# Optimization experiments

Hardware: AMD Instinct MI355X
Metric: run time of the kernel (lower is better)

Reference implementation:

```python
import jax, jax.numpy as jnp
import numpy as np

D_MODEL = 64  # per-head dim used for temperature


def setup_inputs() -> dict:
    key = jax.random.key(0)
    kq, kk, kv, km = jax.random.split(key, 4)
    B, S, D = 16, 2048, D_MODEL
    q = jax.random.normal(kq, (B, S, D), dtype=jnp.float32)
    k = jax.random.normal(kk, (B, S, D), dtype=jnp.float32)
    v = jax.random.normal(kv, (B, S, D), dtype=jnp.float32)
    attn_mask = jax.random.randint(km, (B, S), 0, 2).astype(bool)  # True = masked
    return {"q": q, "k": k, "v": v, "attn_mask": attn_mask}


def reference(q, k, v, attn_mask):
    temper = jnp.asarray(D_MODEL ** 0.5, dtype=q.dtype)
    # scores: [B, S_q, S_k]
    attn = jnp.einsum('bqd,bkd->bqk', q, k) / temper
    # mask broadcast over query dim (torch: unsqueeze(1).expand_as)
    attn = jnp.where(attn_mask[:, None, :], -jnp.inf, attn)
    attn = jax.nn.softmax(attn, axis=-1)
    # nan-fix: fully-masked rows produce NaN -> set to 0 (matches torch code)
    attn = jnp.where(jnp.isnan(attn), jnp.zeros((), dtype=attn.dtype), attn)
    # dropout prob is 0.0 -> identity
    output = jnp.einsum('bqk,bkd->bqd', attn, v)
    return (output, attn)
```

## Files before the change

### kernel.cpp

```cpp
#include <hip/hip_runtime.h>
#include <math.h>

constexpr int B = 16, S = 2048, D = 64;
constexpr int TQ = 128;
constexpr int TK = 64;
constexpr int NT = S / TK;
constexpr float SCALE = 0.125f;
constexpr int STR = 72;

typedef __attribute__((ext_vector_type(8))) short bf16x8;
typedef __attribute__((ext_vector_type(16))) float f32x16;

__device__ __forceinline__ unsigned short f2bf(float x) {
    union { float f; unsigned u; } c; c.f = x;
    return (unsigned short)((c.u + 0x7fff + ((c.u >> 16) & 1)) >> 16);
}
__device__ __forceinline__ float bf2f(unsigned short h) {
    union { unsigned u; float f; } c; c.u = ((unsigned)h) << 16; return c.f;
}
__device__ __forceinline__ unsigned pk2(float a, float b) {
    return (unsigned)f2bf(a) | ((unsigned)f2bf(b) << 16);
}

__global__ __launch_bounds__(256)
void sdpa_mfma(const float* __restrict__ qg, const float* __restrict__ kg,
               const float* __restrict__ vg, const int* __restrict__ maskg,
               float* __restrict__ outg, float* __restrict__ attng)
{
    __shared__ __align__(16) short Qs[TQ * STR];
    __shared__ __align__(16) short Ks[TK * STR];
    __shared__ __align__(16) short Vt[D * STR];
    __shared__ __align__(16) short Ps[4 * 32 * STR];
    __shared__ float mflag[TK];

    const int t = threadIdx.x;
    const int w = t >> 6, lane = t & 63, m = lane & 31, half = lane >> 5;
    const int b = blockIdx.x >> 4;
    const int q0 = (blockIdx.x & 15) * TQ;

    {
        const float4* src = (const float4*)(qg + ((size_t)b * S + q0) * D);
        #pragma unroll
        for (int i = 0; i < 8; ++i) {
            int f4 = t + i * 256;
            float4 v = src[f4];
            int r = f4 >> 4, c = (f4 & 15) * 4;
            unsigned* dst = (unsigned*)&Qs[r * STR + c];
            dst[0] = pk2(v.x, v.y); dst[1] = pk2(v.z, v.w);
        }
    }
    __syncthreads();

    bf16x8 aq[4];
    #pragma unroll
    for (int s = 0; s < 4; ++s)
        aq[s] = *(const bf16x8*)&Qs[(w * 32 + m) * STR + s * 16 + half * 8];

    auto stageK = [&](int gk) {
        const float4* src = (const float4*)(kg + ((size_t)b * S + gk) * D);
        #pragma unroll
        for (int i = 0; i < 4; ++i) {
            int f4 = t + i * 256;
            float4 v = src[f4];
            int r = f4 >> 4, c = (f4 & 15) * 4;
            unsigned* dst = (unsigned*)&Ks[r * STR + c];
            dst[0] = pk2(v.x, v.y); dst[1] = pk2(v.z, v.w);
        }
        if (t < TK) mflag[t] = maskg[b * S + gk + t] ? 1.0f : 0.0f;
    };
    auto stageV = [&](int gk) {
        const float4* src = (const float4*)(vg + ((size_t)b * S + gk) * D);
        #pragma unroll
        for (int i = 0; i < 4; ++i) {
            int f4 = t + i * 256;
            float4 v = src[f4];
            int r = f4 >> 4, c = (f4 & 15) * 4;
            Vt[(c + 0) * STR + r] = (short)f2bf(v.x);
            Vt[(c + 1) * STR + r] = (short)f2bf(v.y);
            Vt[(c + 2) * STR + r] = (short)f2bf(v.z);
            Vt[(c + 3) * STR + r] = (short)f2bf(v.w);
        }
    };
    auto scores = [&](f32x16& c0, f32x16& c1) {
        #pragma unroll
        for (int i = 0; i < 16; ++i) { c0[i] = 0.f; c1[i] = 0.f; }
        #pragma unroll
        for (int s = 0; s < 4; ++s) {
            bf16x8 b0 = *(const bf16x8*)&Ks[m * STR + s * 16 + half * 8];
            bf16x8 b1 = *(const bf16x8*)&Ks[(32 + m) * STR + s * 16 + half * 8];
            c0 = __builtin_amdgcn_mfma_f32_32x32x16_bf16(aq[s], b0, c0, 0, 0, 0);
            c1 = __builtin_amdgcn_mfma_f32_32x32x16_bf16(aq[s], b1, c1, 0, 0, 0);
        }
    };

    float rs[16];
    #pragma unroll
    for (int r = 0; r < 16; ++r) rs[r] = 0.f;

    for (int tile = 0; tile < NT; ++tile) {
        stageK(tile * TK);
        __syncthreads();
        f32x16 c0, c1; scores(c0, c1);
        float mk0 = mflag[m], mk1 = mflag[32 + m];
        #pragma unroll
        for (int r = 0; r < 16; ++r) {
            float p0 = (mk0 == 0.f) ? __expf(c0[r] * SCALE) : 0.f;
            float p1 = (mk1 == 0.f) ? __expf(c1[r] * SCALE) : 0.f;
            rs[r] += p0 + p1;
        }
        __syncthreads();
    }
    #pragma unroll
    for (int off = 1; off < 32; off <<= 1)
        #pragma unroll
        for (int r = 0; r < 16; ++r) rs[r] += __shfl_xor(rs[r], off, 64);
    float rli[16];
    #pragma unroll
    for (int r = 0; r < 16; ++r) rli[r] = rs[r] > 0.f ? 1.f / rs[r] : 0.f;

    f32x16 o0, o1;
    #pragma unroll
    for (int i = 0; i < 16; ++i) { o0[i] = 0.f; o1[i] = 0.f; }
    short* Pw = &Ps[w * 32 * STR];
    float* abase = attng + ((size_t)(b * S + q0 + w * 32)) * S;

    for (int tile = 0; tile < NT; ++tile) {
        const int gk = tile * TK;
        stageK(gk); stageV(gk);
        __syncthreads();
        f32x16 c0, c1; scores(c0, c1);
        float mk0 = mflag[m], mk1 = mflag[32 + m];
        #pragma unroll
        for (int r = 0; r < 16; ++r) {
            int row = (r & 3) + 8 * (r >> 2) + 4 * half;
            float p0 = (mk0 == 0.f) ? __expf(c0[r] * SCALE) * rli[r] : 0.f;
            float p1 = (mk1 == 0.f) ? __expf(c1[r] * SCALE) * rli[r] : 0.f;
            Pw[row * STR + m]      = (short)f2bf(p0);
            Pw[row * STR + 32 + m] = (short)f2bf(p1);
        }
        #pragma unroll
        for (int i = 0; i < 16; ++i) {
            int row = i * 2 + half;
            unsigned u = *(const unsigned*)&Pw[row * STR + 2 * m];
            float2 val = make_float2(bf2f((unsigned short)(u & 0xffff)),
                                     bf2f((unsigned short)(u >> 16)));
            *(float2*)&abase[(size_t)row * S + gk + 2 * m] = val;
        }
        #pragma unroll
        for (int kk = 0; kk < 4; ++kk) {
            bf16x8 ap  = *(const bf16x8*)&Pw[m * STR + kk * 16 + half * 8];
            bf16x8 bv0 = *(const bf16x8*)&Vt[m * STR + kk * 16 + half * 8];
            bf16x8 bv1 = *(const bf16x8*)&Vt[(32 + m) * STR + kk * 16 + half * 8];
            o0 = __builtin_amdgcn_mfma_f32_32x32x16_bf16(ap, bv0, o0, 0, 0, 0);
            o1 = __builtin_amdgcn_mfma_f32_32x32x16_bf16(ap, bv1, o1, 0, 0, 0);
        }
        __syncthreads();
    }

    float* obase = outg + ((size_t)(b * S + q0 + w * 32)) * D;
    #pragma unroll
    for (int r = 0; r < 16; ++r) {
        int row = (r & 3) + 8 * (r >> 2) + 4 * half;
        obase[row * D + m]      = o0[r];
        obase[row * D + 32 + m] = o1[r];
    }
}

extern "C" void kernel_launch(void* const* d_in, const int* in_sizes, int n_in,
                              void* d_out, int out_size, void* d_ws, size_t ws_size,
                              hipStream_t stream) {
    const float* q    = (const float*)d_in[0];
    const float* k    = (const float*)d_in[1];
    const float* v    = (const float*)d_in[2];
    const int*   mask = (const int*)d_in[3];

    float* out  = (float*)d_out;
    float* attn = (float*)d_out + (size_t)B * S * D;

    dim3 grid(B * (S / TQ));
    dim3 block(256);
    sdpa_mfma<<<grid, block, 0, stream>>>(q, k, v, mask, out, attn);
}
```

Before: 420.8 us.

## Preconvert Q/K/V to bf16 in workspace and pipeline 64-row query tiles

A separate pre-pass converts Q and K to bf16 and V to a transposed bf16 layout in the workspace, so the main kernel loads 16-byte bf16 chunks directly instead of converting fp32 on every tile. The main kernel now uses 64-query tiles split across 2x2 waves, with register-staged double-buffered K/V loads that prefetch the next tile during compute. It also writes the attention matrix with coalesced float4 stores through a shared P tile. The old kernel is kept as a fallback when the workspace is too small. The costs are an extra launch, a cross-wave row-sum exchange, and an extra barrier per tile.

```diff
diff --git a/kernel.cpp b/kernel.cpp
--- a/kernel.cpp
+++ b/kernel.cpp
@@ -2,11 +2,10 @@
 #include <math.h>
 
 constexpr int B = 16, S = 2048, D = 64;
-constexpr int TQ = 128;
 constexpr int TK = 64;
 constexpr int NT = S / TK;
 constexpr float SCALE = 0.125f;
-constexpr int STR = 72;
+constexpr int STRH = 88;
 
 typedef __attribute__((ext_vector_type(8))) short bf16x8;
 typedef __attribute__((ext_vector_type(16))) float f32x16;
@@ -21,22 +20,207 @@
 __device__ __forceinline__ unsigned pk2(float a, float b) {
     return (unsigned)f2bf(a) | ((unsigned)f2bf(b) << 16);
 }
+__device__ __forceinline__ int rowof(int h, int r) { return (r & 3) + 8 * (r >> 2) + 4 * h; }
 
 __global__ __launch_bounds__(256)
-void sdpa_mfma(const float* __restrict__ qg, const float* __restrict__ kg,
-               const float* __restrict__ vg, const int* __restrict__ maskg,
-               float* __restrict__ outg, float* __restrict__ attng)
+void preconv(const float* __restrict__ q, const float* __restrict__ k,
+             const float* __restrict__ v, unsigned short* __restrict__ Qb,
+             unsigned short* __restrict__ Kb, unsigned short* __restrict__ Vtb)
 {
-    __shared__ __align__(16) short Qs[TQ * STR];
-    __shared__ __align__(16) short Ks[TK * STR];
-    __shared__ __align__(16) short Vt[D * STR];
-    __shared__ __align__(16) short Ps[4 * 32 * STR];
-    __shared__ float mflag[TK];
+    __shared__ unsigned short vt[64 * 72];
+    const int b = blockIdx.x >> 5, s0 = (blockIdx.x & 31) * 64;
+    const int t = threadIdx.x;
+
+    const float4* qs = (const float4*)(q + ((size_t)b * S + s0) * D);
+    const float4* ks = (const float4*)(k + ((size_t)b * S + s0) * D);
+    const float4* vs = (const float4*)(v + ((size_t)b * S + s0) * D);
+    unsigned* Qd = (unsigned*)(Qb + ((size_t)b * S + s0) * D);
+    unsigned* Kd = (unsigned*)(Kb + ((size_t)b * S + s0) * D);
+
+    #pragma unroll
+    for (int i = 0; i < 4; ++i) {
+        int f4 = t + 256 * i;
+        float4 x = qs[f4];
+        Qd[f4 * 2] = pk2(x.x, x.y); Qd[f4 * 2 + 1] = pk2(x.z, x.w);
+        float4 y = ks[f4];
+        Kd[f4 * 2] = pk2(y.x, y.y); Kd[f4 * 2 + 1] = pk2(y.z, y.w);
+        float4 z = vs[f4];
+        int r = f4 >> 4, cc = (f4 & 15) * 4;
+        vt[(cc + 0) * 72 + r] = f2bf(z.x);
+        vt[(cc + 1) * 72 + r] = f2bf(z.y);
+        vt[(cc + 2) * 72 + r] = f2bf(z.z);
+        vt[(cc + 3) * 72 + r] = f2bf(z.w);
+    }
+    __syncthreads();
+    #pragma unroll
+    for (int i = 0; i < 2; ++i) {
+        int ch = t + 256 * i;
+        int d = ch >> 3, o = ch & 7;
+        int4 val = *(const int4*)&vt[d * 72 + o * 8];
+        *(int4*)(Vtb + ((size_t)(b * 64 + d)) * S + s0 + o * 8) = val;
+    }
+}
+
+__global__ __launch_bounds__(256)
+void sdpa_v3(const unsigned short* __restrict__ Qb, const unsigned short* __restrict__ Kb,
+             const unsigned short* __restrict__ Vtb, const int* __restrict__ maskg,
+             float* __restrict__ outg, float* __restrict__ attng)
+{
+    __shared__ __align__(16) short Ks[2][TK * STRH];
+    __shared__ __align__(16) short Vt[2][TK * STRH];
+    __shared__ __align__(16) short Ps[64 * STRH];
+    __shared__ float mfl[2][TK];
+    __shared__ float rsum[2][64];
+
+    const int t = threadIdx.x;
+    const int w = t >> 6, lane = t & 63, m = lane & 31, h = lane >> 5;
+    const int p = w >> 1, c = w & 1;
+    const int b = blockIdx.x >> 5;
+    const int q0 = (blockIdx.x & 31) * 64;
+
+    bf16x8 aq[4];
+    {
+        const unsigned short* qrow = Qb + ((size_t)(b * S + q0 + 32 * p + m)) * D;
+        #pragma unroll
+        for (int s = 0; s < 4; ++s) aq[s] = *(const bf16x8*)(qrow + s * 16 + h * 8);
+    }
+
+    int4 kreg[2], vreg[2];
+    int mreg = 0;
+
+    auto gloadK = [&](int gk) {
+        #pragma unroll
+        for (int i = 0; i < 2; ++i) {
+            int ch = t + 256 * i;
+            kreg[i] = *(const int4*)(Kb + ((size_t)(b * S + gk + (ch >> 3))) * D + (ch & 7) * 8);
+        }
+        if (t < TK) mreg = maskg[b * S + gk + t];
+    };
+    auto gloadV = [&](int gk) {
+        #pragma unroll
+        for (int i = 0; i < 2; ++i) {
+            int ch = t + 256 * i;
+            vreg[i] = *(const int4*)(Vtb + ((size_t)(b * 64 + (ch >> 3))) * S + gk + (ch & 7) * 8);
+        }
+    };
+    auto commitK = [&](int buf) {
+        #pragma unroll
+        for (int i = 0; i < 2; ++i) {
+            int ch = t + 256 * i;
+            *(int4*)&Ks[buf][(ch >> 3) * STRH + (ch & 7) * 8] = kreg[i];
+        }
+        if (t < TK) mfl[buf][t] = mreg ? 1.0f : 0.0f;
+    };
+    auto commitV = [&](int buf) {
+        #pragma unroll
+        for (int i = 0; i < 2; ++i) {
+            int ch = t + 256 * i;
+            *(int4*)&Vt[buf][(ch >> 3) * STRH + (ch & 7) * 8] = vreg[i];
+        }
+    };
+    auto scores = [&](int buf, f32x16& c0) {
+        #pragma unroll
+        for (int i = 0; i < 16; ++i) c0[i] = 0.f;
+        #pragma unroll
+        for (int s = 0; s < 4; ++s) {
+            bf16x8 bk = *(const bf16x8*)&Ks[buf][(32 * c + m) * STRH + s * 16 + h * 8];
+            c0 = __builtin_amdgcn_mfma_f32_32x32x16_bf16(aq[s], bk, c0, 0, 0, 0);
+        }
+    };
+
+    float rs[16];
+    #pragma unroll
+    for (int r = 0; r < 16; ++r) rs[r] = 0.f;
+
+    gloadK(0);
+    for (int t2 = 0; t2 < NT; ++t2) {
+        commitK(t2 & 1);
+        __syncthreads();
+        if (t2 + 1 < NT) gloadK((t2 + 1) * TK);
+        f32x16 c0; scores(t2 & 1, c0);
+        float mk = mfl[t2 & 1][32 * c + m];
+        #pragma unroll
+        for (int r = 0; r < 16; ++r)
+            if (mk == 0.f) rs[r] += __expf(c0[r] * SCALE);
+    }
+    #pragma unroll
+    for (int off = 1; off < 32; off <<= 1)
+        #pragma unroll
+        for (int r = 0; r < 16; ++r) rs[r] += __shfl_xor(rs[r], off, 64);
+    if (m == 0) {
+        #pragma unroll
+        for (int r = 0; r < 16; ++r) rsum[c][32 * p + rowof(h, r)] = rs[r];
+    }
+    __syncthreads();
+    float rli[16];
+    #pragma unroll
+    for (int r = 0; r < 16; ++r) {
+        int row = 32 * p + rowof(h, r);
+        float tot = rsum[0][row] + rsum[1][row];
+        rli[r] = tot > 0.f ? 1.f / tot : 0.f;
+    }
+
+    f32x16 o;
+    #pragma unroll
+    for (int i = 0; i < 16; ++i) o[i] = 0.f;
+
+    gloadK(0); gloadV(0);
+    for (int t2 = 0; t2 < NT; ++t2) {
+        const int gk = t2 * TK;
+        const int buf = t2 & 1;
+        commitK(buf); commitV(buf);
+        __syncthreads();
+        if (t2 + 1 < NT) { gloadK(gk + TK); gloadV(gk + TK); }
+
+        f32x16 c0; scores(buf, c0);
+        float mk = mfl[buf][32 * c + m];
+        #pragma unroll
+        for (int r = 0; r < 16; ++r) {
+            float pv = (mk == 0.f) ? __expf(c0[r] * SCALE) * rli[r] : 0.f;
+            Ps[(32 * p + rowof(h, r)) * STRH + 32 * c + m] = (short)f2bf(pv);
+        }
+        __syncthreads();
+
+        float* ab = attng + ((size_t)(b * S + q0)) * S + gk;
+        #pragma unroll
+        for (int i = 0; i < 2; ++i) {
+            int ch = t + 256 * i;
+            int rr = ch >> 3, o8 = ch & 7;
+            bf16x8 pv8 = *(const bf16x8*)&Ps[rr * STRH + o8 * 8];
+            float4 f0 = make_float4(bf2f(pv8[0]), bf2f(pv8[1]), bf2f(pv8[2]), bf2f(pv8[3]));
+            float4 f1 = make_float4(bf2f(pv8[4]), bf2f(pv8[5]), bf2f(pv8[6]), bf2f(pv8[7]));
+            float* dst = ab + (size_t)rr * S + o8 * 8;
+            *(float4*)dst = f0; *(float4*)(dst + 4) = f1;
+        }
+        #pragma unroll
+        for (int kk = 0; kk < 4; ++kk) {
+            bf16x8 ap = *(const bf16x8*)&Ps[(32 * p + m) * STRH + kk * 16 + h * 8];
+            bf16x8 bv = *(const bf16x8*)&Vt[buf][(32 * c + m) * STRH + kk * 16 + h * 8];
+            o = __builtin_amdgcn_mfma_f32_32x32x16_bf16(ap, bv, o, 0, 0, 0);
+        }
+    }
+
+    #pragma unroll
+    for (int r = 0; r < 16; ++r)
+        outg[((size_t)(b * S + q0 + 32 * p + rowof(h, r))) * D + 32 * c + m] = o[r];
+}
+
+__global__ __launch_bounds__(256)
+void sdpa_fb(const float* __restrict__ qg, const float* __restrict__ kg,
+             const float* __restrict__ vg, const int* __restrict__ maskg,
+             float* __restrict__ outg, float* __restrict__ attng)
+{
+    constexpr int FSTR = 72;
+    __shared__ __align__(16) short Qs[128 * FSTR];
+    __shared__ __align__(16) short KsF[64 * FSTR];
+    __shared__ __align__(16) short VtF[64 * FSTR];
+    __shared__ __align__(16) short PsF[4 * 32 * FSTR];
+    __shared__ float mflag[64];
 
     const int t = threadIdx.x;
     const int w = t >> 6, lane = t & 63, m = lane & 31, half = lane >> 5;
     const int b = blockIdx.x >> 4;
-    const int q0 = (blockIdx.x & 15) * TQ;
+    const int q0 = (blockIdx.x & 15) * 128;
 
     {
         const float4* src = (const float4*)(qg + ((size_t)b * S + q0) * D);
@@ -44,17 +228,15 @@
         for (int i = 0; i < 8; ++i) {
             int f4 = t + i * 256;
             float4 v = src[f4];
-            int r = f4 >> 4, c = (f4 & 15) * 4;
-            unsigned* dst = (unsigned*)&Qs[r * STR + c];
+            unsigned* dst = (unsigned*)&Qs[(f4 >> 4) * FSTR + (f4 & 15) * 4];
             dst[0] = pk2(v.x, v.y); dst[1] = pk2(v.z, v.w);
         }
     }
     __syncthreads();
-
     bf16x8 aq[4];
     #pragma unroll
     for (int s = 0; s < 4; ++s)
-        aq[s] = *(const bf16x8*)&Qs[(w * 32 + m) * STR + s * 16 + half * 8];
+        aq[s] = *(const bf16x8*)&Qs[(w * 32 + m) * FSTR + s * 16 + half * 8];
 
     auto stageK = [&](int gk) {
         const float4* src = (const float4*)(kg + ((size_t)b * S + gk) * D);
@@ -62,11 +244,10 @@
         for (int i = 0; i < 4; ++i) {
             int f4 = t + i * 256;
             float4 v = src[f4];
-            int r = f4 >> 4, c = (f4 & 15) * 4;
-            unsigned* dst = (unsigned*)&Ks[r * STR + c];
+            unsigned* dst = (unsigned*)&KsF[(f4 >> 4) * FSTR + (f4 & 15) * 4];
             dst[0] = pk2(v.x, v.y); dst[1] = pk2(v.z, v.w);
         }
-        if (t < TK) mflag[t] = maskg[b * S + gk + t] ? 1.0f : 0.0f;
+        if (t < 64) mflag[t] = maskg[b * S + gk + t] ? 1.0f : 0.0f;
     };
     auto stageV = [&](int gk) {
         const float4* src = (const float4*)(vg + ((size_t)b * S + gk) * D);
@@ -74,20 +255,20 @@
         for (int i = 0; i < 4; ++i) {
             int f4 = t + i * 256;
             float4 v = src[f4];
-            int r = f4 >> 4, c = (f4 & 15) * 4;
-            Vt[(c + 0) * STR + r] = (short)f2bf(v.x);
-            Vt[(c + 1) * STR + r] = (short)f2bf(v.y);
-            Vt[(c + 2) * STR + r] = (short)f2bf(v.z);
-            Vt[(c + 3) * STR + r] = (short)f2bf(v.w);
-        }
-    };
-    auto scores = [&](f32x16& c0, f32x16& c1) {
+            int r = f4 >> 4, cc = (f4 & 15) * 4;
+            VtF[(cc + 0) * FSTR + r] = (short)f2bf(v.x);
+            VtF[(cc + 1) * FSTR + r] = (short)f2bf(v.y);
+            VtF[(cc + 2) * FSTR + r] = (short)f2bf(v.z);
+            VtF[(cc + 3) * FSTR + r] = (short)f2bf(v.w);
+        }
+    };
+    auto scoresF = [&](f32x16& c0, f32x16& c1) {
         #pragma unroll
         for (int i = 0; i < 16; ++i) { c0[i] = 0.f; c1[i] = 0.f; }
         #pragma unroll
         for (int s = 0; s < 4; ++s) {
-            bf16x8 b0 = *(const bf16x8*)&Ks[m * STR + s * 16 + half * 8];
-            bf16x8 b1 = *(const bf16x8*)&Ks[(32 + m) * STR + s * 16 + half * 8];
+            bf16x8 b0 = *(const bf16x8*)&KsF[m * FSTR + s * 16 + half * 8];
+            bf16x8 b1 = *(const bf16x8*)&KsF[(32 + m) * FSTR + s * 16 + half * 8];
             c0 = __builtin_amdgcn_mfma_f32_32x32x16_bf16(aq[s], b0, c0, 0, 0, 0);
             c1 = __builtin_amdgcn_mfma_f32_32x32x16_bf16(aq[s], b1, c1, 0, 0, 0);
         }
@@ -96,11 +277,10 @@
     float rs[16];
     #pragma unroll
     for (int r = 0; r < 16; ++r) rs[r] = 0.f;
-
     for (int tile = 0; tile < NT; ++tile) {
         stageK(tile * TK);
         __syncthreads();
-        f32x16 c0, c1; scores(c0, c1);
+        f32x16 c0, c1; scoresF(c0, c1);
         float mk0 = mflag[m], mk1 = mflag[32 + m];
         #pragma unroll
         for (int r = 0; r < 16; ++r) {
@@ -121,46 +301,45 @@
     f32x16 o0, o1;
     #pragma unroll
     for (int i = 0; i < 16; ++i) { o0[i] = 0.f; o1[i] = 0.f; }
-    short* Pw = &Ps[w * 32 * STR];
+    short* Pw = &PsF[w * 32 * FSTR];
     float* abase = attng + ((size_t)(b * S + q0 + w * 32)) * S;
 
     for (int tile = 0; tile < NT; ++tile) {
         const int gk = tile * TK;
         stageK(gk); stageV(gk);
         __syncthreads();
-        f32x16 c0, c1; scores(c0, c1);
+        f32x16 c0, c1; scoresF(c0, c1);
         float mk0 = mflag[m], mk1 = mflag[32 + m];
         #pragma unroll
         for (int r = 0; r < 16; ++r) {
-            int row = (r & 3) + 8 * (r >> 2) + 4 * half;
+            int row = rowof(half, r);
             float p0 = (mk0 == 0.f) ? __expf(c0[r] * SCALE) * rli[r] : 0.f;
             float p1 = (mk1 == 0.f) ? __expf(c1[r] * SCALE) * rli[r] : 0.f;
-            Pw[row * STR + m]      = (short)f2bf(p0);
-            Pw[row * STR + 32 + m] = (short)f2bf(p1);
+            Pw[row * FSTR + m]      = (short)f2bf(p0);
+            Pw[row * FSTR + 32 + m] = (short)f2bf(p1);
         }
         #pragma unroll
         for (int i = 0; i < 16; ++i) {
             int row = i * 2 + half;
-            unsigned u = *(const unsigned*)&Pw[row * STR + 2 * m];
+            unsigned u = *(const unsigned*)&Pw[row * FSTR + 2 * m];
             float2 val = make_float2(bf2f((unsigned short)(u & 0xffff)),
                                      bf2f((unsigned short)(u >> 16)));
             *(float2*)&abase[(size_t)row * S + gk + 2 * m] = val;
         }
         #pragma unroll
         for (int kk = 0; kk < 4; ++kk) {
-            bf16x8 ap  = *(const bf16x8*)&Pw[m * STR + kk * 16 + half * 8];
-            bf16x8 bv0 = *(const bf16x8*)&Vt[m * STR + kk * 16 + half * 8];
-            bf16x8 bv1 = *(const bf16x8*)&Vt[(32 + m) * STR + kk * 16 + half * 8];
+            bf16x8 ap  = *(const bf16x8*)&Pw[m * FSTR + kk * 16 + half * 8];
+            bf16x8 bv0 = *(const bf16x8*)&VtF[m * FSTR + kk * 16 + half * 8];
+            bf16x8 bv1 = *(const bf16x8*)&VtF[(32 + m) * FSTR + kk * 16 + half * 8];
             o0 = __builtin_amdgcn_mfma_f32_32x32x16_bf16(ap, bv0, o0, 0, 0, 0);
             o1 = __builtin_amdgcn_mfma_f32_32x32x16_bf16(ap, bv1, o1, 0, 0, 0);
         }
         __syncthreads();
     }
-
     float* obase = outg + ((size_t)(b * S + q0 + w * 32)) * D;
     #pragma unroll
     for (int r = 0; r < 16; ++r) {
-        int row = (r & 3) + 8 * (r >> 2) + 4 * half;
+        int row = rowof(half, r);
         obase[row * D + m]      = o0[r];
         obase[row * D + 32 + m] = o1[r];
     }
@@ -177,7 +356,16 @@
     float* out  = (float*)d_out;
     float* attn = (float*)d_out + (size_t)B * S * D;
 
-    dim3 grid(B * (S / TQ));
-    dim3 block(256);
-    sdpa_mfma<<<grid, block, 0, stream>>>(q, k, v, mask, out, attn);
-}
+    const size_t elems = (size_t)B * S * D;
+    const size_t need  = 3 * elems * sizeof(unsigned short);
+
+    if (ws_size >= need) {
+        unsigned short* Qb  = (unsigned short*)d_ws;
+        unsigned short* Kb  = Qb + elems;
+        unsigned short* Vtb = Kb + elems;
+        preconv<<<dim3(B * (S / 64)), dim3(256), 0, stream>>>(q, k, v, Qb, Kb, Vtb);
+        sdpa_v3<<<dim3(B * (S / 64)), dim3(256), 0, stream>>>(Qb, Kb, Vtb, mask, out, attn);
+    } else {
+        sdpa_fb<<<dim3(B * (S / 128)), dim3(256), 0, stream>>>(q, k, v, mask, out, attn);
+    }
+}
```

New measurement: 374.7 us. 11.0% less time.
